# Kernel optimization log

Measured on AMD Instinct MI355X. Metric: run time of the kernel, lower is better.

## Reference

```python
import jax, jax.numpy as jnp
import numpy as np

K = 3   # num nearest neighbors (init k)
P = 2   # IDW power (init p)


def setup_inputs() -> dict:
    key = jax.random.key(0)
    k1, k2, k3, k4 = jax.random.split(key, 4)
    B, N, M, C = 8, 16384, 1024, 256
    xyz = jax.random.normal(k1, (B, N, 3), dtype=jnp.float32)
    sampled_xyz = jax.random.normal(k2, (B, M, 3), dtype=jnp.float32)
    sampled_features = jax.random.normal(k3, (B, M, C), dtype=jnp.float32)
    masks = jax.random.randint(k4, (B, N), 0, 2, dtype=jnp.int32)
    return {"xyz": xyz, "sampled_xyz": sampled_xyz,
            "sampled_features": sampled_features, "masks": masks}


def reference(xyz, sampled_xyz, sampled_features, masks):
    # xyz: [B,N,3], sampled_xyz: [B,M,3], sampled_features: [B,M,C], masks: [B,N]
    # Squared pairwise distances [B,N,M] (same math as the chunked torch loop).
    delta = xyz[:, :, None, :] - sampled_xyz[:, None, :, :]
    dists = jnp.sum(delta * delta, axis=-1)
    # k smallest distances -> negate and take top-k.
    neg_top, idx = jax.lax.top_k(-dists, K)          # [B,N,K]
    min_dists = jnp.maximum(-neg_top, 1e-10)
    weights = 1.0 / (min_dists ** P + 1e-10)
    weights = weights / jnp.sum(weights, axis=-1, keepdims=True)
    # Gather neighbor features: [B,N,K,C]
    gathered = jax.vmap(lambda f, i: f[i])(sampled_features, idx)
    interpolated = jnp.sum(gathered * weights[..., None], axis=2)  # [B,N,C]
    # Invalid (masked-out) rows stay zero, matching the padded scatter.
    valid = (masks != 0).astype(interpolated.dtype)
    return interpolated * valid[..., None]
```

## Files before the change

kernel.cpp:

```cpp
#include <hip/hip_runtime.h>

constexpr int B = 8;
constexpr int N = 16384;
constexpr int M = 1024;
constexpr int C = 256;
constexpr int PTS = 64;
constexpr int QW  = 4;

typedef float vf16 __attribute__((ext_vector_type(16)));

__global__ __launch_bounds__(256, 8) void upsample_idw_kernel(
    const float* __restrict__ xyz,
    const float* __restrict__ sxyz,
    const float* __restrict__ feats,
    const int*   __restrict__ masks,
    float*       __restrict__ out)
{
    const int tid = threadIdx.x;
    const int w   = tid >> 6;
    const int l   = tid & 63;
    const int blk = blockIdx.x;
    const int b     = blk & 7;
    const int nbase = (blk >> 3) << 6;

    __shared__ unsigned long long s_key[PTS][QW][3];
    __shared__ float s_w[PTS][3];
    __shared__ int   s_j[PTS][4];

    const float* xp = xyz + ((size_t)b * N + nbase + l) * 3;
    const float x = xp[0], y = xp[1], z = xp[2];

    const float* bbase = sxyz + (size_t)b * (M * 3);
    const int qoff = __builtin_amdgcn_readfirstlane((tid >> 6) * (256 * 12));

    float d0 = __builtin_inff(), d1 = __builtin_inff(), d2 = __builtin_inff();
    int   i0 = 0, i1 = 0, i2 = 0;

    for (int ch = 0; ch < 16; ++ch) {
        vf16 ca, cb, cc;
        const int off = qoff + ch * 192;
        asm volatile(
            "s_load_dwordx16 %0, %3, %4\n\t"
            "s_load_dwordx16 %1, %3, %4 offset:64\n\t"
            "s_load_dwordx16 %2, %3, %4 offset:128\n\t"
            "s_waitcnt lgkmcnt(0)"
            : "=&s"(ca), "=&s"(cb), "=&s"(cc)
            : "s"(bbase), "s"(off));
        #pragma unroll
        for (int j = 0; j < 16; ++j) {
            const int f0 = 3 * j, f1 = 3 * j + 1, f2 = 3 * j + 2;
            const float cx = (f0 < 16) ? ca[f0 & 15] : (f0 < 32) ? cb[f0 & 15] : cc[f0 & 15];
            const float cy = (f1 < 16) ? ca[f1 & 15] : (f1 < 32) ? cb[f1 & 15] : cc[f1 & 15];
            const float cz = (f2 < 16) ? ca[f2 & 15] : (f2 < 32) ? cb[f2 & 15] : cc[f2 & 15];
            const float dx = __fsub_rn(cx, x);
            const float dy = __fsub_rn(cy, y);
            const float dz = __fsub_rn(cz, z);
            const float d  = __fadd_rn(__fadd_rn(__fmul_rn(dx, dx), __fmul_rn(dy, dy)),
                                       __fmul_rn(dz, dz));
            const int m = ch * 16 + j;
            const bool lt0 = d < d0, lt1 = d < d1, lt2 = d < d2;
            i2 = lt1 ? i1 : (lt2 ? m : i2);
            i1 = lt0 ? i0 : (lt1 ? m : i1);
            i0 = lt0 ? m  : i0;
            const float nd2 = __builtin_amdgcn_fmed3f(d1, d2, d);
            const float nd1 = __builtin_amdgcn_fmed3f(d0, d1, d);
            d2 = nd2; d1 = nd1; d0 = fminf(d0, d);
        }
    }

    const unsigned base = (unsigned)(w * 256);
    s_key[l][w][0] = ((unsigned long long)__float_as_uint(d0) << 32) | (base + (unsigned)i0);
    s_key[l][w][1] = ((unsigned long long)__float_as_uint(d1) << 32) | (base + (unsigned)i1);
    s_key[l][w][2] = ((unsigned long long)__float_as_uint(d2) << 32) | (base + (unsigned)i2);
    __syncthreads();

    if (tid < PTS) {
        unsigned long long k0 = ~0ULL, k1 = ~0ULL, k2 = ~0ULL;
        #pragma unroll
        for (int q = 0; q < QW; ++q) {
            #pragma unroll
            for (int s = 0; s < 3; ++s) {
                const unsigned long long k = s_key[tid][q][s];
                const bool lt0 = k < k0, lt1 = k < k1, lt2 = k < k2;
                k2 = lt1 ? k1 : (lt2 ? k : k2);
                k1 = lt0 ? k0 : (lt1 ? k : k1);
                k0 = lt0 ? k  : k0;
            }
        }
        const float e0 = __uint_as_float((unsigned)(k0 >> 32));
        const float e1 = __uint_as_float((unsigned)(k1 >> 32));
        const float e2 = __uint_as_float((unsigned)(k2 >> 32));
        const float m0 = fmaxf(e0, 1e-10f);
        const float m1 = fmaxf(e1, 1e-10f);
        const float m2 = fmaxf(e2, 1e-10f);
        float w0 = 1.0f / (m0 * m0 + 1e-10f);
        float w1 = 1.0f / (m1 * m1 + 1e-10f);
        float w2 = 1.0f / (m2 * m2 + 1e-10f);
        const int valid = masks[(size_t)b * N + nbase + tid];
        const float scale = valid ? (1.0f / (w0 + w1 + w2)) : 0.0f;
        s_w[tid][0] = w0 * scale;
        s_w[tid][1] = w1 * scale;
        s_w[tid][2] = w2 * scale;
        s_j[tid][0] = (int)(unsigned)k0;
        s_j[tid][1] = (int)(unsigned)k1;
        s_j[tid][2] = (int)(unsigned)k2;
        s_j[tid][3] = valid;
    }
    __syncthreads();

    const int pq = tid >> 6;
    const int cq = tid & 63;
    const float4* Fb4 = (const float4*)(feats + (size_t)b * (M * C));
    float4* op4 = (float4*)(out + (((size_t)b * N + nbase) * C));

    for (int p0 = 0; p0 < PTS; p0 += 4) {
        const int p = p0 + pq;
        const int vld = __builtin_amdgcn_readfirstlane(s_j[p][3]);
        float4 acc = make_float4(0.f, 0.f, 0.f, 0.f);
        if (vld) {
            const int j0 = __builtin_amdgcn_readfirstlane(s_j[p][0]);
            const int j1 = __builtin_amdgcn_readfirstlane(s_j[p][1]);
            const int j2 = __builtin_amdgcn_readfirstlane(s_j[p][2]);
            const float w0 = __uint_as_float(
                __builtin_amdgcn_readfirstlane((int)__float_as_uint(s_w[p][0])));
            const float w1 = __uint_as_float(
                __builtin_amdgcn_readfirstlane((int)__float_as_uint(s_w[p][1])));
            const float w2 = __uint_as_float(
                __builtin_amdgcn_readfirstlane((int)__float_as_uint(s_w[p][2])));
            const float4 f0 = Fb4[j0 * 64 + cq];
            const float4 f1 = Fb4[j1 * 64 + cq];
            const float4 f2 = Fb4[j2 * 64 + cq];
            acc.x = fmaf(w2, f2.x, fmaf(w1, f1.x, w0 * f0.x));
            acc.y = fmaf(w2, f2.y, fmaf(w1, f1.y, w0 * f0.y));
            acc.z = fmaf(w2, f2.z, fmaf(w1, f1.z, w0 * f0.z));
            acc.w = fmaf(w2, f2.w, fmaf(w1, f1.w, w0 * f0.w));
        }
        op4[p * 64 + cq] = acc;
    }
}

extern "C" void kernel_launch(void* const* d_in, const int* in_sizes, int n_in,
                              void* d_out, int out_size, void* d_ws, size_t ws_size,
                              hipStream_t stream) {
    const float* xyz   = (const float*)d_in[0];
    const float* sxyz  = (const float*)d_in[1];
    const float* feats = (const float*)d_in[2];
    const int*   masks = (const int*)d_in[3];
    float*       out   = (float*)d_out;

    dim3 grid(B * N / PTS);
    dim3 block(256);
    hipLaunchKernelGGL(upsample_idw_kernel, grid, block, 0, stream,
                       xyz, sxyz, feats, masks, out);
}
```

Measured before the change: 66.24 us.

## Process two point tiles per block, overlapping gather of first with scan of second

```diff
diff --git a/kernel.cpp b/kernel.cpp
--- a/kernel.cpp
+++ b/kernel.cpp
@@ -4,8 +4,7 @@
 constexpr int N = 16384;
 constexpr int M = 1024;
 constexpr int C = 256;
-constexpr int PTS = 64;
-constexpr int QW  = 4;
+constexpr int QW = 4;
 
 typedef float vf16 __attribute__((ext_vector_type(16)));
 
@@ -21,22 +20,27 @@
     const int l   = tid & 63;
     const int blk = blockIdx.x;
     const int b     = blk & 7;
-    const int nbase = (blk >> 3) << 6;
+    const int nbase = (blk >> 3) << 7;
 
-    __shared__ unsigned long long s_key[PTS][QW][3];
-    __shared__ float s_w[PTS][3];
-    __shared__ int   s_j[PTS][4];
-
-    const float* xp = xyz + ((size_t)b * N + nbase + l) * 3;
-    const float x = xp[0], y = xp[1], z = xp[2];
+    __shared__ unsigned long long s_key[2][64][QW][3];
+    __shared__ float s_wt[2][64][3];
+    __shared__ int   s_j[2][64][4];
 
     const float* bbase = sxyz + (size_t)b * (M * 3);
     const int qoff = __builtin_amdgcn_readfirstlane((tid >> 6) * (256 * 12));
 
-    float d0 = __builtin_inff(), d1 = __builtin_inff(), d2 = __builtin_inff();
-    int   i0 = 0, i1 = 0, i2 = 0;
+    const float* xp0 = xyz + ((size_t)b * N + nbase + l) * 3;
+    const float* xp1 = xyz + ((size_t)b * N + nbase + 64 + l) * 3;
+    const float x0 = xp0[0], y0 = xp0[1], z0 = xp0[2];
+    const float x1 = xp1[0], y1 = xp1[1], z1 = xp1[2];
 
-    for (int ch = 0; ch < 16; ++ch) {
+    const float4* Fb4 = (const float4*)(feats + (size_t)b * (M * C));
+    float4* op40 = (float4*)(out + (((size_t)b * N + nbase) * C));
+    float4* op41 = (float4*)(out + (((size_t)b * N + nbase + 64) * C));
+
+    auto scan_chunk = [&](int ch, float px, float py, float pz,
+                          float& d0, float& d1, float& d2,
+                          int& i0, int& i1, int& i2) {
         vf16 ca, cb, cc;
         const int off = qoff + ch * 192;
         asm volatile(
@@ -52,9 +56,9 @@
             const float cx = (f0 < 16) ? ca[f0 & 15] : (f0 < 32) ? cb[f0 & 15] : cc[f0 & 15];
             const float cy = (f1 < 16) ? ca[f1 & 15] : (f1 < 32) ? cb[f1 & 15] : cc[f1 & 15];
             const float cz = (f2 < 16) ? ca[f2 & 15] : (f2 < 32) ? cb[f2 & 15] : cc[f2 & 15];
-            const float dx = __fsub_rn(cx, x);
-            const float dy = __fsub_rn(cy, y);
-            const float dz = __fsub_rn(cz, z);
+            const float dx = __fsub_rn(cx, px);
+            const float dy = __fsub_rn(cy, py);
+            const float dz = __fsub_rn(cz, pz);
             const float d  = __fadd_rn(__fadd_rn(__fmul_rn(dx, dx), __fmul_rn(dy, dy)),
                                        __fmul_rn(dz, dz));
             const int m = ch * 16 + j;
@@ -66,77 +70,102 @@
             const float nd1 = __builtin_amdgcn_fmed3f(d0, d1, d);
             d2 = nd2; d1 = nd1; d0 = fminf(d0, d);
         }
+    };
+
+    auto store_keys = [&](int t, float d0, float d1, float d2,
+                          int i0, int i1, int i2) {
+        const unsigned base = (unsigned)(w * 256);
+        s_key[t][l][w][0] = ((unsigned long long)__float_as_uint(d0) << 32) | (base + (unsigned)i0);
+        s_key[t][l][w][1] = ((unsigned long long)__float_as_uint(d1) << 32) | (base + (unsigned)i1);
+        s_key[t][l][w][2] = ((unsigned long long)__float_as_uint(d2) << 32) | (base + (unsigned)i2);
+    };
+
+    auto merge = [&](int t) {
+        if (tid < 64) {
+            unsigned long long k0 = ~0ULL, k1 = ~0ULL, k2 = ~0ULL;
+            #pragma unroll
+            for (int q = 0; q < QW; ++q) {
+                #pragma unroll
+                for (int s = 0; s < 3; ++s) {
+                    const unsigned long long k = s_key[t][tid][q][s];
+                    const bool lt0 = k < k0, lt1 = k < k1, lt2 = k < k2;
+                    k2 = lt1 ? k1 : (lt2 ? k : k2);
+                    k1 = lt0 ? k0 : (lt1 ? k : k1);
+                    k0 = lt0 ? k  : k0;
+                }
+            }
+            const float e0 = __uint_as_float((unsigned)(k0 >> 32));
+            const float e1 = __uint_as_float((unsigned)(k1 >> 32));
+            const float e2 = __uint_as_float((unsigned)(k2 >> 32));
+            const float m0 = fmaxf(e0, 1e-10f);
+            const float m1 = fmaxf(e1, 1e-10f);
+            const float m2 = fmaxf(e2, 1e-10f);
+            float w0 = 1.0f / (m0 * m0 + 1e-10f);
+            float w1 = 1.0f / (m1 * m1 + 1e-10f);
+            float w2 = 1.0f / (m2 * m2 + 1e-10f);
+            const int valid = masks[(size_t)b * N + nbase + t * 64 + tid];
+            const float scale = valid ? (1.0f / (w0 + w1 + w2)) : 0.0f;
+            s_wt[t][tid][0] = w0 * scale;
+            s_wt[t][tid][1] = w1 * scale;
+            s_wt[t][tid][2] = w2 * scale;
+            s_j[t][tid][0] = (int)(unsigned)k0;
+            s_j[t][tid][1] = (int)(unsigned)k1;
+            s_j[t][tid][2] = (int)(unsigned)k2;
+            s_j[t][tid][3] = valid;
+        }
+    };
+
+    auto phase2_iter = [&](int t, int i, float4* op4) {
+        const int p = 4 * i + w;
+        const int vld = __builtin_amdgcn_readfirstlane(s_j[t][p][3]);
+        float4 acc = make_float4(0.f, 0.f, 0.f, 0.f);
+        if (vld) {
+            const int j0 = __builtin_amdgcn_readfirstlane(s_j[t][p][0]);
+            const int j1 = __builtin_amdgcn_readfirstlane(s_j[t][p][1]);
+            const int j2 = __builtin_amdgcn_readfirstlane(s_j[t][p][2]);
+            const float u0 = __uint_as_float(
+                __builtin_amdgcn_readfirstlane((int)__float_as_uint(s_wt[t][p][0])));
+            const float u1 = __uint_as_float(
+                __builtin_amdgcn_readfirstlane((int)__float_as_uint(s_wt[t][p][1])));
+            const float u2 = __uint_as_float(
+                __builtin_amdgcn_readfirstlane((int)__float_as_uint(s_wt[t][p][2])));
+            const float4 f0 = Fb4[j0 * 64 + l];
+            const float4 f1 = Fb4[j1 * 64 + l];
+            const float4 f2 = Fb4[j2 * 64 + l];
+            acc.x = fmaf(u2, f2.x, fmaf(u1, f1.x, u0 * f0.x));
+            acc.y = fmaf(u2, f2.y, fmaf(u1, f1.y, u0 * f0.y));
+            acc.z = fmaf(u2, f2.z, fmaf(u1, f1.z, u0 * f0.z));
+            acc.w = fmaf(u2, f2.w, fmaf(u1, f1.w, u0 * f0.w));
+        }
+        op4[p * 64 + l] = acc;
+    };
+
+    {
+        float d0 = __builtin_inff(), d1 = __builtin_inff(), d2 = __builtin_inff();
+        int   i0 = 0, i1 = 0, i2 = 0;
+        for (int ch = 0; ch < 16; ++ch)
+            scan_chunk(ch, x0, y0, z0, d0, d1, d2, i0, i1, i2);
+        store_keys(0, d0, d1, d2, i0, i1, i2);
     }
-
-    const unsigned base = (unsigned)(w * 256);
-    s_key[l][w][0] = ((unsigned long long)__float_as_uint(d0) << 32) | (base + (unsigned)i0);
-    s_key[l][w][1] = ((unsigned long long)__float_as_uint(d1) << 32) | (base + (unsigned)i1);
-    s_key[l][w][2] = ((unsigned long long)__float_as_uint(d2) << 32) | (base + (unsigned)i2);
+    __syncthreads();
+    merge(0);
     __syncthreads();
 
-    if (tid < PTS) {
-        unsigned long long k0 = ~0ULL, k1 = ~0ULL, k2 = ~0ULL;
-        #pragma unroll
-        for (int q = 0; q < QW; ++q) {
-            #pragma unroll
-            for (int s = 0; s < 3; ++s) {
-                const unsigned long long k = s_key[tid][q][s];
-                const bool lt0 = k < k0, lt1 = k < k1, lt2 = k < k2;
-                k2 = lt1 ? k1 : (lt2 ? k : k2);
-                k1 = lt0 ? k0 : (lt1 ? k : k1);
-                k0 = lt0 ? k  : k0;
-            }
+    {
+        float d0 = __builtin_inff(), d1 = __builtin_inff(), d2 = __builtin_inff();
+        int   i0 = 0, i1 = 0, i2 = 0;
+        for (int i = 0; i < 16; ++i) {
+            phase2_iter(0, i, op40);
+            scan_chunk(i, x1, y1, z1, d0, d1, d2, i0, i1, i2);
         }
-        const float e0 = __uint_as_float((unsigned)(k0 >> 32));
-        const float e1 = __uint_as_float((unsigned)(k1 >> 32));
-        const float e2 = __uint_as_float((unsigned)(k2 >> 32));
-        const float m0 = fmaxf(e0, 1e-10f);
-        const float m1 = fmaxf(e1, 1e-10f);
-        const float m2 = fmaxf(e2, 1e-10f);
-        float w0 = 1.0f / (m0 * m0 + 1e-10f);
-        float w1 = 1.0f / (m1 * m1 + 1e-10f);
-        float w2 = 1.0f / (m2 * m2 + 1e-10f);
-        const int valid = masks[(size_t)b * N + nbase + tid];
-        const float scale = valid ? (1.0f / (w0 + w1 + w2)) : 0.0f;
-        s_w[tid][0] = w0 * scale;
-        s_w[tid][1] = w1 * scale;
-        s_w[tid][2] = w2 * scale;
-        s_j[tid][0] = (int)(unsigned)k0;
-        s_j[tid][1] = (int)(unsigned)k1;
-        s_j[tid][2] = (int)(unsigned)k2;
-        s_j[tid][3] = valid;
+        store_keys(1, d0, d1, d2, i0, i1, i2);
     }
     __syncthreads();
+    merge(1);
+    __syncthreads();
 
-    const int pq = tid >> 6;
-    const int cq = tid & 63;
-    const float4* Fb4 = (const float4*)(feats + (size_t)b * (M * C));
-    float4* op4 = (float4*)(out + (((size_t)b * N + nbase) * C));
-
-    for (int p0 = 0; p0 < PTS; p0 += 4) {
-        const int p = p0 + pq;
-        const int vld = __builtin_amdgcn_readfirstlane(s_j[p][3]);
-        float4 acc = make_float4(0.f, 0.f, 0.f, 0.f);
-        if (vld) {
-            const int j0 = __builtin_amdgcn_readfirstlane(s_j[p][0]);
-            const int j1 = __builtin_amdgcn_readfirstlane(s_j[p][1]);
-            const int j2 = __builtin_amdgcn_readfirstlane(s_j[p][2]);
-            const float w0 = __uint_as_float(
-                __builtin_amdgcn_readfirstlane((int)__float_as_uint(s_w[p][0])));
-            const float w1 = __uint_as_float(
-                __builtin_amdgcn_readfirstlane((int)__float_as_uint(s_w[p][1])));
-            const float w2 = __uint_as_float(
-                __builtin_amdgcn_readfirstlane((int)__float_as_uint(s_w[p][2])));
-            const float4 f0 = Fb4[j0 * 64 + cq];
-            const float4 f1 = Fb4[j1 * 64 + cq];
-            const float4 f2 = Fb4[j2 * 64 + cq];
-            acc.x = fmaf(w2, f2.x, fmaf(w1, f1.x, w0 * f0.x));
-            acc.y = fmaf(w2, f2.y, fmaf(w1, f1.y, w0 * f0.y));
-            acc.z = fmaf(w2, f2.z, fmaf(w1, f1.z, w0 * f0.z));
-            acc.w = fmaf(w2, f2.w, fmaf(w1, f1.w, w0 * f0.w));
-        }
-        op4[p * 64 + cq] = acc;
-    }
+    for (int i = 0; i < 16; ++i)
+        phase2_iter(1, i, op41);
 }
 
 extern "C" void kernel_launch(void* const* d_in, const int* in_sizes, int n_in,
@@ -148,7 +177,7 @@
     const int*   masks = (const int*)d_in[3];
     float*       out   = (float*)d_out;
 
-    dim3 grid(B * N / PTS);
+    dim3 grid(B * N / 128);
     dim3 block(256);
     hipLaunchKernelGGL(upsample_idw_kernel, grid, block, 0, stream,
                        xyz, sxyz, feats, masks, out);
```

Result: slower. 80.51 us (+21.5%).

## Transpose sampled xyz to SoA and compute distances with packed f32 ops

Applied to the files above, without the earlier changes.

```diff
diff --git a/kernel.cpp b/kernel.cpp
--- a/kernel.cpp
+++ b/kernel.cpp
@@ -9,9 +9,21 @@
 
 typedef float vf16 __attribute__((ext_vector_type(16)));
 
+__global__ __launch_bounds__(256) void transpose_sxyz_kernel(
+    const float* __restrict__ sxyz, float* __restrict__ ws)
+{
+    const int g = blockIdx.x * 256 + threadIdx.x;
+    const int b = g >> 10, m = g & 1023;
+    float* o = ws + b * 3072;
+    const float* s = sxyz + (size_t)g * 3;
+    o[m]        = s[0];
+    o[1024 + m] = s[1];
+    o[2048 + m] = s[2];
+}
+
 __global__ __launch_bounds__(256, 8) void upsample_idw_kernel(
     const float* __restrict__ xyz,
-    const float* __restrict__ sxyz,
+    const float* __restrict__ ws,
     const float* __restrict__ feats,
     const int*   __restrict__ masks,
     float*       __restrict__ out)
@@ -29,42 +41,55 @@
 
     const float* xp = xyz + ((size_t)b * N + nbase + l) * 3;
     const float x = xp[0], y = xp[1], z = xp[2];
+    float2 px2; px2.x = x; px2.y = x;
+    float2 py2; py2.x = y; py2.y = y;
+    float2 pz2; pz2.x = z; pz2.y = z;
 
-    const float* bbase = sxyz + (size_t)b * (M * 3);
-    const int qoff = __builtin_amdgcn_readfirstlane((tid >> 6) * (256 * 12));
+    const float* wsbase = ws + (size_t)b * 3072;
+    const int qoff = __builtin_amdgcn_readfirstlane((tid >> 6) * 1024);
 
     float d0 = __builtin_inff(), d1 = __builtin_inff(), d2 = __builtin_inff();
     int   i0 = 0, i1 = 0, i2 = 0;
 
     for (int ch = 0; ch < 16; ++ch) {
-        vf16 ca, cb, cc;
-        const int off = qoff + ch * 192;
+        vf16 xs, ys, zs;
+        const int off = qoff + ch * 64;
         asm volatile(
             "s_load_dwordx16 %0, %3, %4\n\t"
-            "s_load_dwordx16 %1, %3, %4 offset:64\n\t"
-            "s_load_dwordx16 %2, %3, %4 offset:128\n\t"
+            "s_load_dwordx16 %1, %3, %4 offset:0x1000\n\t"
+            "s_load_dwordx16 %2, %3, %4 offset:0x2000\n\t"
             "s_waitcnt lgkmcnt(0)"
-            : "=&s"(ca), "=&s"(cb), "=&s"(cc)
-            : "s"(bbase), "s"(off));
+            : "=&s"(xs), "=&s"(ys), "=&s"(zs)
+            : "s"(wsbase), "s"(off));
         #pragma unroll
-        for (int j = 0; j < 16; ++j) {
-            const int f0 = 3 * j, f1 = 3 * j + 1, f2 = 3 * j + 2;
-            const float cx = (f0 < 16) ? ca[f0 & 15] : (f0 < 32) ? cb[f0 & 15] : cc[f0 & 15];
-            const float cy = (f1 < 16) ? ca[f1 & 15] : (f1 < 32) ? cb[f1 & 15] : cc[f1 & 15];
-            const float cz = (f2 < 16) ? ca[f2 & 15] : (f2 < 32) ? cb[f2 & 15] : cc[f2 & 15];
-            const float dx = __fsub_rn(cx, x);
-            const float dy = __fsub_rn(cy, y);
-            const float dz = __fsub_rn(cz, z);
-            const float d  = __fadd_rn(__fadd_rn(__fmul_rn(dx, dx), __fmul_rn(dy, dy)),
-                                       __fmul_rn(dz, dz));
-            const int m = ch * 16 + j;
-            const bool lt0 = d < d0, lt1 = d < d1, lt2 = d < d2;
-            i2 = lt1 ? i1 : (lt2 ? m : i2);
-            i1 = lt0 ? i0 : (lt1 ? m : i1);
-            i0 = lt0 ? m  : i0;
-            const float nd2 = __builtin_amdgcn_fmed3f(d1, d2, d);
-            const float nd1 = __builtin_amdgcn_fmed3f(d0, d1, d);
-            d2 = nd2; d1 = nd1; d0 = fminf(d0, d);
+        for (int j = 0; j < 8; ++j) {
+            float2 sx2; sx2.x = xs[2 * j]; sx2.y = xs[2 * j + 1];
+            float2 sy2; sy2.x = ys[2 * j]; sy2.y = ys[2 * j + 1];
+            float2 sz2; sz2.x = zs[2 * j]; sz2.y = zs[2 * j + 1];
+            float2 d01, t0, t1;
+            asm("v_pk_add_f32 %1, %3, %6 neg_lo:[0,1] neg_hi:[0,1]\n\t"
+                "v_pk_mul_f32 %1, %1, %1\n\t"
+                "v_pk_add_f32 %2, %4, %7 neg_lo:[0,1] neg_hi:[0,1]\n\t"
+                "v_pk_mul_f32 %2, %2, %2\n\t"
+                "v_pk_add_f32 %1, %1, %2\n\t"
+                "v_pk_add_f32 %2, %5, %8 neg_lo:[0,1] neg_hi:[0,1]\n\t"
+                "v_pk_mul_f32 %2, %2, %2\n\t"
+                "v_pk_add_f32 %0, %1, %2"
+                : "=&v"(d01), "=&v"(t0), "=&v"(t1)
+                : "s"(sx2), "s"(sy2), "s"(sz2),
+                  "v"(px2), "v"(py2), "v"(pz2));
+            #pragma unroll
+            for (int h = 0; h < 2; ++h) {
+                const float d = (h == 0) ? d01.x : d01.y;
+                const int m = ch * 16 + 2 * j + h;
+                const bool lt0 = d < d0, lt1 = d < d1, lt2 = d < d2;
+                i2 = lt1 ? i1 : (lt2 ? m : i2);
+                i1 = lt0 ? i0 : (lt1 ? m : i1);
+                i0 = lt0 ? m  : i0;
+                const float nd2 = __builtin_amdgcn_fmed3f(d1, d2, d);
+                const float nd1 = __builtin_amdgcn_fmed3f(d0, d1, d);
+                d2 = nd2; d1 = nd1; d0 = fminf(d0, d);
+            }
         }
     }
 
@@ -147,9 +172,13 @@
     const float* feats = (const float*)d_in[2];
     const int*   masks = (const int*)d_in[3];
     float*       out   = (float*)d_out;
+    float*       ws    = (float*)d_ws;
+
+    hipLaunchKernelGGL(transpose_sxyz_kernel, dim3(B * M / 256), dim3(256),
+                       0, stream, sxyz, ws);
 
     dim3 grid(B * N / PTS);
     dim3 block(256);
     hipLaunchKernelGGL(upsample_idw_kernel, grid, block, 0, stream,
-                       xyz, sxyz, feats, masks, out);
+                       xyz, ws, feats, masks, out);
 }
```

Measured after the change: 76.99 us. 16.2% more time.
